# Kernel optimization log

Measured on AMD Instinct MI355X. Metric: run time of the kernel, lower is better.

The kernel has to match this reference:

```python
import jax, jax.numpy as jnp
import numpy as np

N = 2048      # num_nodes (padded graph size)
D = 128       # node_embedding_dim
E = 8         # edge_embedding_dim (num learned edge-type channels)
ITERS = 8     # GGNN iterations (shared weights)


def setup_inputs() -> dict:
    key = jax.random.key(0)
    ks = jax.random.split(key, 8)
    s = 1.0 / np.sqrt(D)
    return {
        "node_embeddings": jax.random.normal(ks[0], (N, D), jnp.float32),
        # dense edge tensor; scaled by 1/N so the sum-over-senders message
        # aggregation stays O(1) in magnitude (real graphs are sparse)
        "edge_embeddings": jax.random.uniform(ks[1], (N, N, E), jnp.float32) / N,
        "W_msg": jax.random.normal(ks[2], (E, D, D), jnp.float32) * s,
        "b_msg": jnp.zeros((D,), jnp.float32),
        "Wi": jax.random.normal(ks[3], (D, 3 * D), jnp.float32) * s,
        "Wh": jax.random.normal(ks[4], (D, 3 * D), jnp.float32) * s,
        "b_gru": jnp.zeros((3 * D,), jnp.float32),
        "A_readout": jax.random.normal(ks[5], (D, D), jnp.float32) * s,
    }


def reference(node_embeddings, edge_embeddings, W_msg, b_msg, Wi, Wh, b_gru, A_readout):
    """GGNN steps (LinearMessagePassing + GRU update, weights shared via scan)
    followed by pairwise bilinear edge readout -> [N, N] logits."""

    def step(h, _):
        # per-edge-type linear transform of sender embeddings: [N, E, D]
        per_edge = jnp.einsum('sd,edh->seh', h, W_msg)
        # aggregate over senders weighted by dense edge tensor: [N, D]
        messages = jnp.einsum('ste,seh->th', edge_embeddings, per_edge) + b_msg
        # gated recurrent (GRU) update: state = node embeddings, input = messages
        gi = messages @ Wi + b_gru            # [N, 3D]
        gh = h @ Wh                           # [N, 3D]
        i_r, i_z, i_n = jnp.split(gi, 3, axis=-1)
        h_r, h_z, h_n = jnp.split(gh, 3, axis=-1)
        r = jax.nn.sigmoid(i_r + h_r)
        z = jax.nn.sigmoid(i_z + h_z)
        n = jnp.tanh(i_n + r * h_n)
        h_new = (1.0 - z) * n + z * h
        return h_new, None

    h, _ = jax.lax.scan(step, node_embeddings, None, length=ITERS)
    # bilinear pairwise readout -> weighted adjacency logits [N, N]
    logits = jnp.einsum('id,de,je->ij', h, A_readout, h)
    return logits
```

## Files before the change

### kernel.cpp

```cpp
#include <hip/hip_runtime.h>
#include <math.h>
#include <stdint.h>

#define Nn 2048
#define Dd 128
#define Ee 8
#define NIT 8
#define KT (Nn*Ee)
#define KSPLIT 16

typedef __bf16 bf16;
typedef __attribute__((ext_vector_type(8))) __bf16 bf16x8;
typedef __attribute__((ext_vector_type(4))) float f32x4;
typedef __attribute__((ext_vector_type(16))) float f32x16;

__device__ __forceinline__ f32x4 mfma16(bf16x8 a, bf16x8 b, f32x4 c){
    return __builtin_amdgcn_mfma_f32_16x16x32_bf16(a, b, c, 0, 0, 0);
}
__device__ __forceinline__ f32x16 mfma32(bf16x8 a, bf16x8 b, f32x16 c){
    return __builtin_amdgcn_mfma_f32_32x32x16_bf16(a, b, c, 0, 0, 0);
}
__device__ __forceinline__ void g2lds16(const void* g, void* l){
    __builtin_amdgcn_global_load_lds((const uint32_t*)g, (uint32_t*)l, 16, 0, 0);
}

__global__ __launch_bounds__(256) void k_prep(
    const float* __restrict__ node, const float* __restrict__ Wmsg,
    const float* __restrict__ Wi,   const float* __restrict__ Wh,
    const float* __restrict__ Ar,
    float* __restrict__ h32, bf16* __restrict__ hb,
    bf16* __restrict__ WmT, bf16* __restrict__ WiT, bf16* __restrict__ WhT,
    bf16* __restrict__ ArT)
{
    int tid = blockIdx.x*256 + threadIdx.x;
    int stride = gridDim.x*256;
    for (int i = tid; i < Nn*Dd; i += stride){
        float v = node[i]; h32[i] = v; hb[i] = (bf16)v;
    }
    for (int i = tid; i < Ee*Dd*Dd; i += stride){
        int e = i >> 14; int r = i & 16383; int h = r >> 7; int d = r & 127;
        WmT[i] = (bf16)Wmsg[e*Dd*Dd + d*Dd + h];
    }
    for (int i = tid; i < 384*Dd; i += stride){
        int j = i >> 7; int d = i & 127;
        WiT[i] = (bf16)Wi[d*384 + j];
        WhT[i] = (bf16)Wh[d*384 + j];
    }
    for (int i = tid; i < Dd*Dd; i += stride){
        int h = i >> 7; int d = i & 127;
        ArT[i] = (bf16)Ar[d*Dd + h];
    }
}

__global__ __launch_bounds__(256) void k_prep_edge(
    const float* __restrict__ edge, bf16* __restrict__ edge_bf)
{
    const size_t total = (size_t)Nn*Nn*Ee;
    size_t base = ((size_t)blockIdx.x*256 + threadIdx.x)*8;
    size_t stride = (size_t)gridDim.x*256*8;
    for (size_t i = base; i < total; i += stride){
        f32x4 v0 = *(const f32x4*)&edge[i];
        f32x4 v1 = *(const f32x4*)&edge[i+4];
        bf16x8 o;
        for (int j = 0; j < 4; j++){ o[j] = (bf16)v0[j]; o[j+4] = (bf16)v1[j]; }
        *(bf16x8*)&edge_bf[i] = o;
    }
}

__global__ __launch_bounds__(256) void k_per_edge(
    const bf16* __restrict__ hb, const bf16* __restrict__ WmT,
    bf16* __restrict__ Pt)
{
    __shared__ bf16 Blds[Ee][16][Dd+8];
    const int s0 = blockIdx.x * 64;
    const int h0 = blockIdx.y * 16;
    const int tid = threadIdx.x;
    for (int i = 0; i < 8; i++){
        int idx = tid + i*256;
        int e = idx >> 8, row = (idx >> 4) & 15, c = idx & 15;
        *(bf16x8*)&Blds[e][row][c*8] =
            *(const bf16x8*)&WmT[e*Dd*Dd + (h0+row)*Dd + c*8];
    }
    __syncthreads();
    const int lane = tid & 63, wave = tid >> 6;
    const int quad = lane >> 4, l16 = lane & 15;
    const int srow = s0 + wave*16 + l16;
    f32x4 acc[Ee];
    for (int e = 0; e < Ee; e++) acc[e] = (f32x4){0.f,0.f,0.f,0.f};
    for (int kk = 0; kk < 4; kk++){
        int k0 = kk*32 + quad*8;
        bf16x8 a = *(const bf16x8*)&hb[srow*Dd + k0];
        for (int e = 0; e < Ee; e++){
            bf16x8 b = *(const bf16x8*)&Blds[e][l16][k0];
            acc[e] = mfma16(a, b, acc[e]);
        }
    }
    const int h = h0 + l16;
    for (int r = 0; r < 4; r++){
        int s = s0 + wave*16 + quad*4 + r;
        bf16x8 po;
        for (int e = 0; e < Ee; e++) po[e] = (bf16)acc[e][r];
        *(bf16x8*)&Pt[((size_t)s*Dd + h)*Ee] = po;
    }
}

__global__ __launch_bounds__(256) void k_msg_gemm(
    const bf16* __restrict__ edge_bf, const bf16* __restrict__ Pt,
    float* __restrict__ msgP)
{
    __shared__ __align__(16) char ldsb[65536];
    const int flat = blockIdx.y*16 + blockIdx.x;
    const int by = (flat & 7)*2 + ((flat >> 3) & 1);
    const int bx = flat >> 4;
    const int t0 = bx * 128;
    const int sblk = by * 128;
    const int tid = threadIdx.x;
    const int lane = tid & 63, wave = tid >> 6;
    const int half = lane >> 5, l31 = lane & 31;
    const int trow = t0 + wave*32 + l31;
    const char* Ptb = (const char*)Pt;

    f32x16 acc[4];
    #pragma unroll
    for (int nt = 0; nt < 4; nt++)
        for (int i = 0; i < 16; i++) acc[nt][i] = 0.f;

    bf16x8 A0[8], A1[8];

#define STAGE(ch_) do{                                                         \
    const char* _src = Ptb + (size_t)(sblk + (ch_)*16)*2048                    \
                           + wave*1024 + lane*16;                              \
    char* _dst = ldsb + ((ch_)&1)*32768 + wave*1024;                           \
    for (int j = 0; j < 8; j++)                                                \
        g2lds16(_src + j*4096, _dst + j*4096);                                 \
}while(0)

#define PREF(AD_, ch_) do{                                                     \
    int _sc = sblk + (ch_)*16 + half;                                          \
    _Pragma("unroll")                                                          \
    for (int ks = 0; ks < 8; ks++)                                             \
        AD_[ks] = *(const bf16x8*)&edge_bf[(size_t)(_sc + ks*2)*16384 + trow*8]; \
}while(0)

#define COMPUTE(AD_, ch_) do{                                                  \
    const bf16* _bt = (const bf16*)(ldsb + ((ch_)&1)*32768);                   \
    _Pragma("unroll")                                                          \
    for (int ks = 0; ks < 8; ks++){                                            \
        const bf16* _bp = _bt + (ks*2 + half)*1024 + l31*8;                    \
        acc[0] = mfma32(AD_[ks], *(const bf16x8*)(_bp      ), acc[0]);         \
        acc[1] = mfma32(AD_[ks], *(const bf16x8*)(_bp + 256), acc[1]);         \
        acc[2] = mfma32(AD_[ks], *(const bf16x8*)(_bp + 512), acc[2]);         \
        acc[3] = mfma32(AD_[ks], *(const bf16x8*)(_bp + 768), acc[3]);         \
    }                                                                          \
}while(0)

    STAGE(0); PREF(A0, 0);
    asm volatile("s_waitcnt vmcnt(0)" ::: "memory");
    __syncthreads();
    #pragma unroll
    for (int cc = 0; cc < 4; cc++){
        const int ch = cc*2;
        STAGE(ch+1); PREF(A1, ch+1);
        COMPUTE(A0, ch);
        asm volatile("s_waitcnt vmcnt(0)" ::: "memory");
        __syncthreads();
        if (ch+2 < 8){ STAGE(ch+2); PREF(A0, ch+2); }
        COMPUTE(A1, ch+1);
        if (ch+2 < 8){
            asm volatile("s_waitcnt vmcnt(0)" ::: "memory");
            __syncthreads();
        }
    }
#undef STAGE
#undef PREF
#undef COMPUTE

    float* dst = msgP + (size_t)by*(Nn*Dd);
    #pragma unroll
    for (int nt = 0; nt < 4; nt++){
        int h = nt*32 + l31;
        #pragma unroll
        for (int r = 0; r < 16; r++){
            int row = (r&3) + 8*(r>>2) + 4*half;
            dst[(size_t)(t0 + wave*32 + row)*Dd + h] = acc[nt][r];
        }
    }
}

__global__ __launch_bounds__(256) void k_msg_reduce(
    const float* __restrict__ msgP, const float* __restrict__ bmsg,
    bf16* __restrict__ msgb)
{
    const int base = (blockIdx.x*256 + threadIdx.x)*8;
    const int d0 = base & (Dd-1);
    f32x4 s0 = *(const f32x4*)&bmsg[d0];
    f32x4 s1 = *(const f32x4*)&bmsg[d0+4];
    #pragma unroll
    for (int p = 0; p < KSPLIT; p++){
        const float* mp = &msgP[(size_t)p*Nn*Dd + base];
        s0 += *(const f32x4*)&mp[0];
        s1 += *(const f32x4*)&mp[4];
    }
    bf16x8 o;
    #pragma unroll
    for (int j = 0; j < 4; j++){ o[j] = (bf16)s0[j]; o[j+4] = (bf16)s1[j]; }
    *(bf16x8*)&msgb[base] = o;
}

__global__ __launch_bounds__(256) void k_gru(
    const bf16* __restrict__ msgb, const bf16* __restrict__ WiT,
    const bf16* __restrict__ WhT, const float* __restrict__ bgru,
    float* __restrict__ h32, bf16* __restrict__ hb)
{
    __shared__ __align__(16) bf16 stage[384][40];
    __shared__ float Gs[16][384];
    __shared__ float Ghn[16][128];

    const int t0 = blockIdx.x * 16;
    const int tid = threadIdx.x;
    const int lane = tid & 63, wave = tid >> 6;
    const int quad = lane >> 4, l16 = lane & 15;

    f32x4 accA[6], accB[6];
    for (int i = 0; i < 6; i++){ accA[i] = (f32x4){0.f,0.f,0.f,0.f}; accB[i] = (f32x4){0.f,0.f,0.f,0.f}; }

    for (int mat = 0; mat < 2; mat++){
        const bf16* WT = mat == 0 ? WiT : WhT;
        for (int kc = 0; kc < 4; kc++){
            for (int i = 0; i < 6; i++){
                int idx = tid + i*256; int row = idx >> 2, c = idx & 3;
                *(bf16x8*)&stage[row][c*8] = *(const bf16x8*)&WT[row*Dd + kc*32 + c*8];
            }
            __syncthreads();
            int k0 = kc*32 + quad*8;
            bf16x8 a;
            if (mat == 0) a = *(const bf16x8*)&msgb[(t0 + l16)*Dd + k0];
            else          a = *(const bf16x8*)&hb  [(t0 + l16)*Dd + k0];
            for (int tt = 0; tt < 6; tt++){
                int T = wave*6 + tt;
                bf16x8 b = *(const bf16x8*)&stage[T*16 + l16][quad*8];
                if (mat == 0 || T < 16) accA[tt] = mfma16(a, b, accA[tt]);
                else                    accB[tt] = mfma16(a, b, accB[tt]);
            }
            __syncthreads();
        }
    }
    for (int tt = 0; tt < 6; tt++){
        int T = wave*6 + tt;
        int j = T*16 + l16;
        for (int r = 0; r < 4; r++){
            int m = quad*4 + r;
            Gs[m][j] = accA[tt][r];
            if (T >= 16) Ghn[m][j - 256] = accB[tt][r];
        }
    }
    __syncthreads();
    for (int i = 0; i < 8; i++){
        int cell = tid + i*256;
        int m = cell >> 7, jd = cell & 127;
        int t = t0 + m;
        float xr = Gs[m][jd]       + bgru[jd];
        float xz = Gs[m][jd + 128] + bgru[jd + 128];
        float xn = Gs[m][jd + 256] + bgru[jd + 256];
        float r = 1.f / (1.f + expf(-xr));
        float z = 1.f / (1.f + expf(-xz));
        float n = tanhf(xn + r * Ghn[m][jd]);
        float ho = h32[t*Dd + jd];
        float hnew = (1.f - z) * n + z * ho;
        h32[t*Dd + jd] = hnew;
        hb [t*Dd + jd] = (bf16)hnew;
    }
}

__global__ __launch_bounds__(256) void k_read1(
    const bf16* __restrict__ hb, const bf16* __restrict__ ArT, bf16* __restrict__ t1)
{
    __shared__ bf16 Blds[Dd][Dd+8];
    const int s0 = blockIdx.x * 64;
    const int tid = threadIdx.x;
    for (int i = 0; i < 8; i++){
        int idx = tid + i*256; int row = idx >> 4, c = idx & 15;
        *(bf16x8*)&Blds[row][c*8] = *(const bf16x8*)&ArT[row*Dd + c*8];
    }
    __syncthreads();
    const int lane = tid & 63, wave = tid >> 6;
    const int quad = lane >> 4, l16 = lane & 15;
    const int srow = s0 + wave*16 + l16;
    f32x4 acc[8];
    for (int nt = 0; nt < 8; nt++) acc[nt] = (f32x4){0.f,0.f,0.f,0.f};
    for (int kk = 0; kk < 4; kk++){
        int k0 = kk*32 + quad*8;
        bf16x8 a = *(const bf16x8*)&hb[srow*Dd + k0];
        for (int nt = 0; nt < 8; nt++){
            bf16x8 b = *(const bf16x8*)&Blds[nt*16 + l16][k0];
            acc[nt] = mfma16(a, b, acc[nt]);
        }
    }
    for (int nt = 0; nt < 8; nt++){
        int h = nt*16 + l16;
        for (int r = 0; r < 4; r++){
            int s = s0 + wave*16 + quad*4 + r;
            t1[s*Dd + h] = (bf16)acc[nt][r];
        }
    }
}

__global__ __launch_bounds__(256) void k_read2(
    const bf16* __restrict__ t1, const bf16* __restrict__ hb, float* __restrict__ out)
{
    const int i0 = blockIdx.x * 64, j0 = blockIdx.y * 128;
    const int tid = threadIdx.x;
    const int lane = tid & 63, wave = tid >> 6;
    const int quad = lane >> 4, l16 = lane & 15;
    const int irow = i0 + wave*16 + l16;
    f32x4 acc[8];
    for (int nt = 0; nt < 8; nt++) acc[nt] = (f32x4){0.f,0.f,0.f,0.f};
    for (int kk = 0; kk < 4; kk++){
        int k0 = kk*32 + quad*8;
        bf16x8 a = *(const bf16x8*)&t1[irow*Dd + k0];
        for (int nt = 0; nt < 8; nt++){
            int j = j0 + nt*16 + l16;
            bf16x8 b = *(const bf16x8*)&hb[j*Dd + k0];
            acc[nt] = mfma16(a, b, acc[nt]);
        }
    }
    for (int nt = 0; nt < 8; nt++){
        int j = j0 + nt*16 + l16;
        for (int r = 0; r < 4; r++){
            int irw = i0 + wave*16 + quad*4 + r;
            out[(size_t)irw*Nn + j] = acc[nt][r];
        }
    }
}

extern "C" void kernel_launch(void* const* d_in, const int* in_sizes, int n_in,
                              void* d_out, int out_size, void* d_ws, size_t ws_size,
                              hipStream_t stream)
{
    const float* node = (const float*)d_in[0];
    const float* edge = (const float*)d_in[1];
    const float* Wmsg = (const float*)d_in[2];
    const float* bmsg = (const float*)d_in[3];
    const float* Wi   = (const float*)d_in[4];
    const float* Wh   = (const float*)d_in[5];
    const float* bgru = (const float*)d_in[6];
    const float* Ar   = (const float*)d_in[7];
    float* out = (float*)d_out;

    char* ws = (char*)d_ws;
    bf16*  edge_bf = (bf16*)ws;          ws += (size_t)Nn*Nn*Ee*2;
    float* msgP = (float*)ws;            ws += (size_t)KSPLIT*Nn*Dd*4;
    bf16*  Pt  = (bf16*)ws;              ws += (size_t)Dd*KT*2;
    float* h32 = (float*)ws;             ws += (size_t)Nn*Dd*4;
    bf16*  hb  = (bf16*)ws;              ws += (size_t)Nn*Dd*2;
    bf16*  WmT = (bf16*)ws;              ws += (size_t)Ee*Dd*Dd*2;
    bf16*  WiT = (bf16*)ws;              ws += (size_t)384*Dd*2;
    bf16*  WhT = (bf16*)ws;              ws += (size_t)384*Dd*2;
    bf16*  ArT = (bf16*)ws;              ws += (size_t)Dd*Dd*2;
    bf16*  t1  = (bf16*)ws;              ws += (size_t)Nn*Dd*2;
    bf16*  msgb = t1;

    k_prep<<<dim3(256), 256, 0, stream>>>(node, Wmsg, Wi, Wh, Ar,
                                          h32, hb, WmT, WiT, WhT, ArT);
    k_prep_edge<<<dim3(4096), 256, 0, stream>>>(edge, edge_bf);
    for (int it = 0; it < NIT; it++){
        k_per_edge <<<dim3(32, 8), 256, 0, stream>>>(hb, WmT, Pt);
        k_msg_gemm <<<dim3(16,16), 256, 0, stream>>>(edge_bf, Pt, msgP);
        k_msg_reduce<<<dim3(128),  256, 0, stream>>>(msgP, bmsg, msgb);
        k_gru      <<<dim3(128),   256, 0, stream>>>(msgb, WiT, WhT, bgru, h32, hb);
    }
    k_read1<<<dim3(32),     256, 0, stream>>>(hb, ArT, t1);
    k_read2<<<dim3(32, 16), 256, 0, stream>>>(t1, hb, out);
}
```

Baseline: 584.9 us.

## Fuse split-K reduce, GRU, and per-edge transform; triple-buffer message GEMM

```diff
diff --git a/kernel.cpp b/kernel.cpp
--- a/kernel.cpp
+++ b/kernel.cpp
@@ -11,6 +11,7 @@
 
 typedef __bf16 bf16;
 typedef __attribute__((ext_vector_type(8))) __bf16 bf16x8;
+typedef __attribute__((ext_vector_type(4))) __bf16 bf16x4;
 typedef __attribute__((ext_vector_type(4))) float f32x4;
 typedef __attribute__((ext_vector_type(16))) float f32x16;
 
@@ -104,11 +105,11 @@
     }
 }
 
-__global__ __launch_bounds__(256) void k_msg_gemm(
+__global__ __launch_bounds__(256, 1) void k_msg_gemm(
     const bf16* __restrict__ edge_bf, const bf16* __restrict__ Pt,
     float* __restrict__ msgP)
 {
-    __shared__ __align__(16) char ldsb[65536];
+    __shared__ __align__(16) char ldsb[3*32768];
     const int flat = blockIdx.y*16 + blockIdx.x;
     const int by = (flat & 7)*2 + ((flat >> 3) & 1);
     const int bx = flat >> 4;
@@ -125,55 +126,61 @@
     for (int nt = 0; nt < 4; nt++)
         for (int i = 0; i < 16; i++) acc[nt][i] = 0.f;
 
-    bf16x8 A0[8], A1[8];
+    bf16x8 A[3][8];
 
 #define STAGE(ch_) do{                                                         \
     const char* _src = Ptb + (size_t)(sblk + (ch_)*16)*2048                    \
                            + wave*1024 + lane*16;                              \
-    char* _dst = ldsb + ((ch_)&1)*32768 + wave*1024;                           \
+    char* _dst = ldsb + ((ch_)%3)*32768 + wave*1024;                           \
+    _Pragma("unroll")                                                          \
     for (int j = 0; j < 8; j++)                                                \
         g2lds16(_src + j*4096, _dst + j*4096);                                 \
 }while(0)
 
-#define PREF(AD_, ch_) do{                                                     \
+#define PREF(ch_) do{                                                         \
     int _sc = sblk + (ch_)*16 + half;                                          \
     _Pragma("unroll")                                                          \
     for (int ks = 0; ks < 8; ks++)                                             \
-        AD_[ks] = *(const bf16x8*)&edge_bf[(size_t)(_sc + ks*2)*16384 + trow*8]; \
+        A[(ch_)%3][ks] = *(const bf16x8*)&edge_bf[(size_t)(_sc + ks*2)*16384 + trow*8]; \
 }while(0)
 
-#define COMPUTE(AD_, ch_) do{                                                  \
-    const bf16* _bt = (const bf16*)(ldsb + ((ch_)&1)*32768);                   \
+#define COMPUTE(ch_) do{                                                       \
+    const bf16* _bt = (const bf16*)(ldsb + ((ch_)%3)*32768);                   \
     _Pragma("unroll")                                                          \
     for (int ks = 0; ks < 8; ks++){                                            \
         const bf16* _bp = _bt + (ks*2 + half)*1024 + l31*8;                    \
-        acc[0] = mfma32(AD_[ks], *(const bf16x8*)(_bp      ), acc[0]);         \
-        acc[1] = mfma32(AD_[ks], *(const bf16x8*)(_bp + 256), acc[1]);         \
-        acc[2] = mfma32(AD_[ks], *(const bf16x8*)(_bp + 512), acc[2]);         \
-        acc[3] = mfma32(AD_[ks], *(const bf16x8*)(_bp + 768), acc[3]);         \
+        acc[0] = mfma32(A[(ch_)%3][ks], *(const bf16x8*)(_bp      ), acc[0]);  \
+        acc[1] = mfma32(A[(ch_)%3][ks], *(const bf16x8*)(_bp + 256), acc[1]);  \
+        acc[2] = mfma32(A[(ch_)%3][ks], *(const bf16x8*)(_bp + 512), acc[2]);  \
+        acc[3] = mfma32(A[(ch_)%3][ks], *(const bf16x8*)(_bp + 768), acc[3]);  \
     }                                                                          \
 }while(0)
 
-    STAGE(0); PREF(A0, 0);
-    asm volatile("s_waitcnt vmcnt(0)" ::: "memory");
-    __syncthreads();
-    #pragma unroll
-    for (int cc = 0; cc < 4; cc++){
-        const int ch = cc*2;
-        STAGE(ch+1); PREF(A1, ch+1);
-        COMPUTE(A0, ch);
-        asm volatile("s_waitcnt vmcnt(0)" ::: "memory");
-        __syncthreads();
-        if (ch+2 < 8){ STAGE(ch+2); PREF(A0, ch+2); }
-        COMPUTE(A1, ch+1);
-        if (ch+2 < 8){
-            asm volatile("s_waitcnt vmcnt(0)" ::: "memory");
-            __syncthreads();
-        }
-    }
+#define STEP(ch_, wcnt_, dostage_) do{                                         \
+    asm volatile("s_waitcnt vmcnt(" #wcnt_ ")" ::: "memory");                  \
+    __builtin_amdgcn_s_barrier();                                              \
+    COMPUTE(ch_);                                                              \
+    __builtin_amdgcn_s_barrier();                                              \
+    if (dostage_){ STAGE((ch_)+3); PREF((ch_)+3); }                            \
+}while(0)
+
+    STAGE(0); PREF(0);
+    STAGE(1); PREF(1);
+    STAGE(2); PREF(2);
+
+    STEP(0, 32, 1);
+    STEP(1, 32, 1);
+    STEP(2, 32, 1);
+    STEP(3, 32, 1);
+    STEP(4, 32, 1);
+    STEP(5, 32, 0);
+    STEP(6, 16, 0);
+    STEP(7,  0, 0);
+
 #undef STAGE
 #undef PREF
 #undef COMPUTE
+#undef STEP
 
     float* dst = msgP + (size_t)by*(Nn*Dd);
     #pragma unroll
@@ -187,88 +194,133 @@
     }
 }
 
-__global__ __launch_bounds__(256) void k_msg_reduce(
+__global__ __launch_bounds__(256) void k_update(
     const float* __restrict__ msgP, const float* __restrict__ bmsg,
-    bf16* __restrict__ msgb)
-{
-    const int base = (blockIdx.x*256 + threadIdx.x)*8;
-    const int d0 = base & (Dd-1);
-    f32x4 s0 = *(const f32x4*)&bmsg[d0];
-    f32x4 s1 = *(const f32x4*)&bmsg[d0+4];
-    #pragma unroll
-    for (int p = 0; p < KSPLIT; p++){
-        const float* mp = &msgP[(size_t)p*Nn*Dd + base];
-        s0 += *(const f32x4*)&mp[0];
-        s1 += *(const f32x4*)&mp[4];
-    }
-    bf16x8 o;
-    #pragma unroll
-    for (int j = 0; j < 4; j++){ o[j] = (bf16)s0[j]; o[j+4] = (bf16)s1[j]; }
-    *(bf16x8*)&msgb[base] = o;
-}
-
-__global__ __launch_bounds__(256) void k_gru(
-    const bf16* __restrict__ msgb, const bf16* __restrict__ WiT,
-    const bf16* __restrict__ WhT, const float* __restrict__ bgru,
-    float* __restrict__ h32, bf16* __restrict__ hb)
-{
-    __shared__ __align__(16) bf16 stage[384][40];
-    __shared__ float Gs[16][384];
-    __shared__ float Ghn[16][128];
-
-    const int t0 = blockIdx.x * 16;
+    const bf16* __restrict__ WiT,  const bf16* __restrict__ WhT,
+    const float* __restrict__ bgru, const bf16* __restrict__ WmT,
+    float* __restrict__ h32, bf16* __restrict__ hb, bf16* __restrict__ Pt)
+{
+    __shared__ __align__(16) bf16 msg_b[16][152];
+    __shared__ __align__(16) bf16 h_b[16][152];
+    __shared__ __align__(16) bf16 hn_b[16][152];
+    __shared__ __align__(16) float Gi[8][388];
+    __shared__ __align__(16) float Gh[8][388];
+
+    const int t0 = blockIdx.x * 8;
     const int tid = threadIdx.x;
     const int lane = tid & 63, wave = tid >> 6;
     const int quad = lane >> 4, l16 = lane & 15;
 
-    f32x4 accA[6], accB[6];
-    for (int i = 0; i < 6; i++){ accA[i] = (f32x4){0.f,0.f,0.f,0.f}; accB[i] = (f32x4){0.f,0.f,0.f,0.f}; }
-
-    for (int mat = 0; mat < 2; mat++){
-        const bf16* WT = mat == 0 ? WiT : WhT;
-        for (int kc = 0; kc < 4; kc++){
-            for (int i = 0; i < 6; i++){
-                int idx = tid + i*256; int row = idx >> 2, c = idx & 3;
-                *(bf16x8*)&stage[row][c*8] = *(const bf16x8*)&WT[row*Dd + kc*32 + c*8];
+    for (int i = tid; i < 8*152; i += 256){
+        (&msg_b[8][0])[i] = (bf16)0.f;
+        (&h_b [8][0])[i] = (bf16)0.f;
+        (&hn_b[8][0])[i] = (bf16)0.f;
+    }
+
+    {
+        int m = tid >> 5;
+        int d0 = (tid & 31) * 4;
+        f32x4 s = *(const f32x4*)&bmsg[d0];
+        #pragma unroll
+        for (int p = 0; p < KSPLIT; p++)
+            s += *(const f32x4*)&msgP[((size_t)p*Nn + t0 + m)*Dd + d0];
+        for (int j = 0; j < 4; j++) msg_b[m][d0+j] = (bf16)s[j];
+        *(bf16x4*)&h_b[m][d0] = *(const bf16x4*)&hb[(t0+m)*Dd + d0];
+    }
+    __syncthreads();
+
+    {
+        f32x4 accA[12];
+        #pragma unroll
+        for (int i = 0; i < 12; i++) accA[i] = (f32x4){0.f,0.f,0.f,0.f};
+        #pragma unroll
+        for (int kk = 0; kk < 4; kk++){
+            int k0 = kk*32 + quad*8;
+            bf16x8 aGi = *(const bf16x8*)&msg_b[l16][k0];
+            bf16x8 aGh = *(const bf16x8*)&h_b[l16][k0];
+            #pragma unroll
+            for (int i = 0; i < 12; i++){
+                int tile = wave*12 + i;
+                int isGi = tile < 24;
+                int jt = isGi ? tile : tile - 24;
+                const bf16* WT = isGi ? WiT : WhT;
+                bf16x8 b = *(const bf16x8*)&WT[(jt*16 + l16)*Dd + k0];
+                accA[i] = mfma16(isGi ? aGi : aGh, b, accA[i]);
             }
-            __syncthreads();
-            int k0 = kc*32 + quad*8;
-            bf16x8 a;
-            if (mat == 0) a = *(const bf16x8*)&msgb[(t0 + l16)*Dd + k0];
-            else          a = *(const bf16x8*)&hb  [(t0 + l16)*Dd + k0];
-            for (int tt = 0; tt < 6; tt++){
-                int T = wave*6 + tt;
-                bf16x8 b = *(const bf16x8*)&stage[T*16 + l16][quad*8];
-                if (mat == 0 || T < 16) accA[tt] = mfma16(a, b, accA[tt]);
-                else                    accB[tt] = mfma16(a, b, accB[tt]);
+        }
+        #pragma unroll
+        for (int i = 0; i < 12; i++){
+            int tile = wave*12 + i;
+            int jt = tile < 24 ? tile : tile - 24;
+            float* G = tile < 24 ? &Gi[0][0] : &Gh[0][0];
+            #pragma unroll
+            for (int r = 0; r < 4; r++){
+                int row = quad*4 + r;
+                if (row < 8) G[row*388 + jt*16 + l16] = accA[i][r];
             }
-            __syncthreads();
-        }
-    }
-    for (int tt = 0; tt < 6; tt++){
-        int T = wave*6 + tt;
-        int j = T*16 + l16;
-        for (int r = 0; r < 4; r++){
-            int m = quad*4 + r;
-            Gs[m][j] = accA[tt][r];
-            if (T >= 16) Ghn[m][j - 256] = accB[tt][r];
         }
     }
     __syncthreads();
-    for (int i = 0; i < 8; i++){
-        int cell = tid + i*256;
-        int m = cell >> 7, jd = cell & 127;
-        int t = t0 + m;
-        float xr = Gs[m][jd]       + bgru[jd];
-        float xz = Gs[m][jd + 128] + bgru[jd + 128];
-        float xn = Gs[m][jd + 256] + bgru[jd + 256];
-        float r = 1.f / (1.f + expf(-xr));
-        float z = 1.f / (1.f + expf(-xz));
-        float n = tanhf(xn + r * Ghn[m][jd]);
-        float ho = h32[t*Dd + jd];
-        float hnew = (1.f - z) * n + z * ho;
-        h32[t*Dd + jd] = hnew;
-        hb [t*Dd + jd] = (bf16)hnew;
+
+    {
+        int m = tid >> 5;
+        int d0 = (tid & 31) * 4;
+        f32x4 gir = *(const f32x4*)&Gi[m][d0];
+        f32x4 giz = *(const f32x4*)&Gi[m][128+d0];
+        f32x4 gin = *(const f32x4*)&Gi[m][256+d0];
+        f32x4 ghr = *(const f32x4*)&Gh[m][d0];
+        f32x4 ghz = *(const f32x4*)&Gh[m][128+d0];
+        f32x4 ghn = *(const f32x4*)&Gh[m][256+d0];
+        f32x4 bR = *(const f32x4*)&bgru[d0];
+        f32x4 bZ = *(const f32x4*)&bgru[128+d0];
+        f32x4 bN = *(const f32x4*)&bgru[256+d0];
+        f32x4 ho = *(const f32x4*)&h32[(t0+m)*Dd + d0];
+        f32x4 hnv; bf16x4 hb4;
+        for (int j = 0; j < 4; j++){
+            float r = 1.f / (1.f + expf(-(gir[j] + ghr[j] + bR[j])));
+            float z = 1.f / (1.f + expf(-(giz[j] + ghz[j] + bZ[j])));
+            float n = tanhf(gin[j] + bN[j] + r * ghn[j]);
+            hnv[j] = (1.f - z) * n + z * ho[j];
+            hb4[j] = (bf16)hnv[j];
+        }
+        *(f32x4*)&h32[(t0+m)*Dd + d0] = hnv;
+        *(bf16x4*)&hb[(t0+m)*Dd + d0] = hb4;
+        *(bf16x4*)&hn_b[m][d0] = hb4;
+    }
+    __syncthreads();
+
+    {
+        f32x4 accP[2][8];
+        #pragma unroll
+        for (int i = 0; i < 2; i++)
+            for (int e = 0; e < 8; e++) accP[i][e] = (f32x4){0.f,0.f,0.f,0.f};
+        #pragma unroll
+        for (int kk = 0; kk < 4; kk++){
+            int k0 = kk*32 + quad*8;
+            bf16x8 a = *(const bf16x8*)&hn_b[l16][k0];
+            #pragma unroll
+            for (int i = 0; i < 2; i++){
+                int th = wave*2 + i;
+                #pragma unroll
+                for (int e = 0; e < 8; e++){
+                    bf16x8 b = *(const bf16x8*)&WmT[e*Dd*Dd + (th*16 + l16)*Dd + k0];
+                    accP[i][e] = mfma16(a, b, accP[i][e]);
+                }
+            }
+        }
+        #pragma unroll
+        for (int i = 0; i < 2; i++){
+            int h = (wave*2 + i)*16 + l16;
+            #pragma unroll
+            for (int r = 0; r < 4; r++){
+                int s = quad*4 + r;
+                if (s < 8){
+                    bf16x8 po;
+                    for (int e = 0; e < 8; e++) po[e] = (bf16)accP[i][e][r];
+                    *(bf16x8*)&Pt[((size_t)(t0 + s)*Dd + h)*Ee] = po;
+                }
+            }
+        }
     }
 }
 
@@ -358,16 +410,15 @@
     bf16*  WhT = (bf16*)ws;              ws += (size_t)384*Dd*2;
     bf16*  ArT = (bf16*)ws;              ws += (size_t)Dd*Dd*2;
     bf16*  t1  = (bf16*)ws;              ws += (size_t)Nn*Dd*2;
-    bf16*  msgb = t1;
 
     k_prep<<<dim3(256), 256, 0, stream>>>(node, Wmsg, Wi, Wh, Ar,
                                           h32, hb, WmT, WiT, WhT, ArT);
     k_prep_edge<<<dim3(4096), 256, 0, stream>>>(edge, edge_bf);
+    k_per_edge<<<dim3(32, 8), 256, 0, stream>>>(hb, WmT, Pt);
     for (int it = 0; it < NIT; it++){
-        k_per_edge <<<dim3(32, 8), 256, 0, stream>>>(hb, WmT, Pt);
-        k_msg_gemm <<<dim3(16,16), 256, 0, stream>>>(edge_bf, Pt, msgP);
-        k_msg_reduce<<<dim3(128),  256, 0, stream>>>(msgP, bmsg, msgb);
-        k_gru      <<<dim3(128),   256, 0, stream>>>(msgb, WiT, WhT, bgru, h32, hb);
+        k_msg_gemm<<<dim3(16,16), 256, 0, stream>>>(edge_bf, Pt, msgP);
+        k_update  <<<dim3(256),   256, 0, stream>>>(msgP, bmsg, WiT, WhT, bgru,
+                                                    WmT, h32, hb, Pt);
     }
     k_read1<<<dim3(32),     256, 0, stream>>>(hb, ArT, t1);
     k_read2<<<dim3(32, 16), 256, 0, stream>>>(t1, hb, out);
```

Result: slower. 628.4 us (+7.4%).

## Fuse edge fp32-to-bf16 conversion into first message GEMM and store partials in bf16

Applied to the files above, without the earlier changes.

```diff
diff --git a/kernel.cpp b/kernel.cpp
--- a/kernel.cpp
+++ b/kernel.cpp
@@ -11,6 +11,7 @@
 
 typedef __bf16 bf16;
 typedef __attribute__((ext_vector_type(8))) __bf16 bf16x8;
+typedef __attribute__((ext_vector_type(4))) __bf16 bf16x4;
 typedef __attribute__((ext_vector_type(4))) float f32x4;
 typedef __attribute__((ext_vector_type(16))) float f32x16;
 
@@ -49,21 +50,6 @@
     for (int i = tid; i < Dd*Dd; i += stride){
         int h = i >> 7; int d = i & 127;
         ArT[i] = (bf16)Ar[d*Dd + h];
-    }
-}
-
-__global__ __launch_bounds__(256) void k_prep_edge(
-    const float* __restrict__ edge, bf16* __restrict__ edge_bf)
-{
-    const size_t total = (size_t)Nn*Nn*Ee;
-    size_t base = ((size_t)blockIdx.x*256 + threadIdx.x)*8;
-    size_t stride = (size_t)gridDim.x*256*8;
-    for (size_t i = base; i < total; i += stride){
-        f32x4 v0 = *(const f32x4*)&edge[i];
-        f32x4 v1 = *(const f32x4*)&edge[i+4];
-        bf16x8 o;
-        for (int j = 0; j < 4; j++){ o[j] = (bf16)v0[j]; o[j+4] = (bf16)v1[j]; }
-        *(bf16x8*)&edge_bf[i] = o;
     }
 }
 
@@ -104,9 +90,10 @@
     }
 }
 
+template<int FIRST>
 __global__ __launch_bounds__(256) void k_msg_gemm(
-    const bf16* __restrict__ edge_bf, const bf16* __restrict__ Pt,
-    float* __restrict__ msgP)
+    const float* __restrict__ edge_f, bf16* __restrict__ edge_bf,
+    const bf16* __restrict__ Pt, bf16* __restrict__ msgP)
 {
     __shared__ __align__(16) char ldsb[65536];
     const int flat = blockIdx.y*16 + blockIdx.x;
@@ -131,6 +118,7 @@
     const char* _src = Ptb + (size_t)(sblk + (ch_)*16)*2048                    \
                            + wave*1024 + lane*16;                              \
     char* _dst = ldsb + ((ch_)&1)*32768 + wave*1024;                           \
+    _Pragma("unroll")                                                          \
     for (int j = 0; j < 8; j++)                                                \
         g2lds16(_src + j*4096, _dst + j*4096);                                 \
 }while(0)
@@ -138,8 +126,21 @@
 #define PREF(AD_, ch_) do{                                                     \
     int _sc = sblk + (ch_)*16 + half;                                          \
     _Pragma("unroll")                                                          \
-    for (int ks = 0; ks < 8; ks++)                                             \
-        AD_[ks] = *(const bf16x8*)&edge_bf[(size_t)(_sc + ks*2)*16384 + trow*8]; \
+    for (int ks = 0; ks < 8; ks++){                                            \
+        size_t _off = (size_t)(_sc + ks*2)*16384 + trow*8;                     \
+        if (FIRST){                                                            \
+            f32x4 _v0 = *(const f32x4*)&edge_f[_off];                          \
+            f32x4 _v1 = *(const f32x4*)&edge_f[_off+4];                        \
+            bf16x8 _o;                                                         \
+            for (int _j = 0; _j < 4; _j++){                                    \
+                _o[_j] = (bf16)_v0[_j]; _o[_j+4] = (bf16)_v1[_j];              \
+            }                                                                  \
+            AD_[ks] = _o;                                                      \
+            *(bf16x8*)&edge_bf[_off] = _o;                                     \
+        } else {                                                               \
+            AD_[ks] = *(const bf16x8*)&edge_bf[_off];                          \
+        }                                                                      \
+    }                                                                          \
 }while(0)
 
 #define COMPUTE(AD_, ch_) do{                                                  \
@@ -175,20 +176,20 @@
 #undef PREF
 #undef COMPUTE
 
-    float* dst = msgP + (size_t)by*(Nn*Dd);
+    bf16* dst = msgP + (size_t)by*(Nn*Dd);
     #pragma unroll
     for (int nt = 0; nt < 4; nt++){
         int h = nt*32 + l31;
         #pragma unroll
         for (int r = 0; r < 16; r++){
             int row = (r&3) + 8*(r>>2) + 4*half;
-            dst[(size_t)(t0 + wave*32 + row)*Dd + h] = acc[nt][r];
+            dst[(size_t)(t0 + wave*32 + row)*Dd + h] = (bf16)acc[nt][r];
         }
     }
 }
 
 __global__ __launch_bounds__(256) void k_msg_reduce(
-    const float* __restrict__ msgP, const float* __restrict__ bmsg,
+    const bf16* __restrict__ msgP, const float* __restrict__ bmsg,
     bf16* __restrict__ msgb)
 {
     const int base = (blockIdx.x*256 + threadIdx.x)*8;
@@ -197,9 +198,12 @@
     f32x4 s1 = *(const f32x4*)&bmsg[d0+4];
     #pragma unroll
     for (int p = 0; p < KSPLIT; p++){
-        const float* mp = &msgP[(size_t)p*Nn*Dd + base];
-        s0 += *(const f32x4*)&mp[0];
-        s1 += *(const f32x4*)&mp[4];
+        bf16x8 v = *(const bf16x8*)&msgP[(size_t)p*Nn*Dd + base];
+        #pragma unroll
+        for (int j = 0; j < 4; j++){
+            s0[j] += (float)v[j];
+            s1[j] += (float)v[j+4];
+        }
     }
     bf16x8 o;
     #pragma unroll
@@ -349,7 +353,7 @@
 
     char* ws = (char*)d_ws;
     bf16*  edge_bf = (bf16*)ws;          ws += (size_t)Nn*Nn*Ee*2;
-    float* msgP = (float*)ws;            ws += (size_t)KSPLIT*Nn*Dd*4;
+    bf16*  msgP = (bf16*)ws;             ws += (size_t)KSPLIT*Nn*Dd*2;
     bf16*  Pt  = (bf16*)ws;              ws += (size_t)Dd*KT*2;
     float* h32 = (float*)ws;             ws += (size_t)Nn*Dd*4;
     bf16*  hb  = (bf16*)ws;              ws += (size_t)Nn*Dd*2;
@@ -362,12 +366,14 @@
 
     k_prep<<<dim3(256), 256, 0, stream>>>(node, Wmsg, Wi, Wh, Ar,
                                           h32, hb, WmT, WiT, WhT, ArT);
-    k_prep_edge<<<dim3(4096), 256, 0, stream>>>(edge, edge_bf);
     for (int it = 0; it < NIT; it++){
-        k_per_edge <<<dim3(32, 8), 256, 0, stream>>>(hb, WmT, Pt);
-        k_msg_gemm <<<dim3(16,16), 256, 0, stream>>>(edge_bf, Pt, msgP);
-        k_msg_reduce<<<dim3(128),  256, 0, stream>>>(msgP, bmsg, msgb);
-        k_gru      <<<dim3(128),   256, 0, stream>>>(msgb, WiT, WhT, bgru, h32, hb);
+        k_per_edge<<<dim3(32, 8), 256, 0, stream>>>(hb, WmT, Pt);
+        if (it == 0)
+            k_msg_gemm<1><<<dim3(16,16), 256, 0, stream>>>(edge, edge_bf, Pt, msgP);
+        else
+            k_msg_gemm<0><<<dim3(16,16), 256, 0, stream>>>(edge, edge_bf, Pt, msgP);
+        k_msg_reduce<<<dim3(128), 256, 0, stream>>>(msgP, bmsg, msgb);
+        k_gru<<<dim3(128), 256, 0, stream>>>(msgb, WiT, WhT, bgru, h32, hb);
     }
     k_read1<<<dim3(32),     256, 0, stream>>>(hb, ArT, t1);
     k_read2<<<dim3(32, 16), 256, 0, stream>>>(t1, hb, out);
```

Result: faster. 567.0 us (-3.1%).
